# Optimization experiments

Hardware: AMD Instinct MI355X
Metric: run time of the kernel (lower is better)

The kernel has to match this reference:

```python
import jax, jax.numpy as jnp
import numpy as np

K = 16      # n_sample neighbors
L = 2       # stacked PT blocks
D = 128     # in_dim
H = 128     # hidden_dim = out_dim = vector_dim
EPS = 1e-5


def _bn(x, g, b, axes):
    # batch-norm with batch statistics (train-mode MinkowskiBatchNorm / BN1d / BN2d)
    m = jnp.mean(x, axes, keepdims=True)
    v = jnp.var(x, axes, keepdims=True)
    return (x - m) * jax.lax.rsqrt(v + EPS) * g + b


def setup_inputs():
    key = jax.random.key(0)
    ks = jax.random.split(key, 16)
    B, Nper = 2, 8192
    coords = jax.random.randint(ks[0], (B, Nper, 3), 0, 200, dtype=jnp.int32)
    feats = jax.random.normal(ks[1], (B * Nper, D), dtype=jnp.float32)
    w = lambda k, s: jax.random.normal(k, s, dtype=jnp.float32) * 0.1
    return {
        'coords': coords, 'feats': feats,
        'W_top': w(ks[2], (L, D, H)),
        'bn_top_g': jnp.ones((L, H)), 'bn_top_b': jnp.zeros((L, H)),
        'W_phi': w(ks[3], (L, H, H)),
        'W_psi': w(ks[4], (L, H, H)),
        'W_alpha': w(ks[5], (L, H, H)),
        'W_d1': w(ks[6], (L, 3, H)), 'b_d1': jnp.zeros((L, H)),
        'bn_d1_g': jnp.ones((L, H)), 'bn_d1_b': jnp.zeros((L, H)),
        'W_d2': w(ks[7], (L, H, H)), 'b_d2': jnp.zeros((L, H)),
        'bn_d2_g': jnp.ones((L, H)), 'bn_d2_b': jnp.zeros((L, H)),
        'W_g1': w(ks[8], (L, H, H)), 'b_g1': jnp.zeros((L, H)),
        'bn_g1_g': jnp.ones((L, H)), 'bn_g1_b': jnp.zeros((L, H)),
        'W_g2': w(ks[9], (L, H, H)), 'b_g2': jnp.zeros((L, H)),
        'bn_g2_g': jnp.ones((L, H)), 'bn_g2_b': jnp.zeros((L, H)),
        'W_down': w(ks[10], (L, H, D)),
        'bn_down_g': jnp.ones((L, D)), 'bn_down_b': jnp.zeros((L, D)),
    }


def _knn(coords):
    # cube_query with USE_KNN=True: per-scene KNN grouping (self included)
    cf = coords.astype(jnp.float32)

    def one(c):  # c: (Nper, 3)
        d2 = jnp.sum((c[:, None, :] - c[None, :, :]) ** 2, -1)  # (Nper, Nper)
        _, idx = jax.lax.top_k(-d2, K)
        return idx

    idx = jax.vmap(one)(cf)                      # (B, Nper, K) per-scene indices
    nbr = jax.vmap(lambda c, i: c[i])(cf, idx)   # (B, Nper, K, 3) grouped coords
    rel = nbr - cf[:, :, None, :]                # relative xyz (pose input)
    B, Nper = coords.shape[0], coords.shape[1]
    gidx = (idx + (jnp.arange(B, dtype=idx.dtype) * Nper)[:, None, None]).reshape(-1, K)
    return rel.reshape(-1, K, 3), gidx           # (N,K,3), (N,K) global indices


def reference(coords, feats, W_top, bn_top_g, bn_top_b, W_phi, W_psi, W_alpha,
              W_d1, b_d1, bn_d1_g, bn_d1_b, W_d2, b_d2, bn_d2_g, bn_d2_b,
              W_g1, b_g1, bn_g1_g, bn_g1_b, W_g2, b_g2, bn_g2_g, bn_g2_b,
              W_down, bn_down_g, bn_down_b):
    rel, gidx = _knn(coords)
    f = feats
    for l in range(L):
        h = _bn(f @ W_top[l], bn_top_g[l], bn_top_b[l], 0)  # linear_top (1x1 conv + BN)
        # delta: pointwise MLP 3 -> H -> H on relative xyz (position encoding)
        pose = jax.nn.relu(_bn(rel @ W_d1[l] + b_d1[l], bn_d1_g[l], bn_d1_b[l], (0, 1)))
        pose = _bn(pose @ W_d2[l] + b_d2[l], bn_d2_g[l], bn_d2_b[l], (0, 1))  # (N,K,H)
        q = h @ W_phi[l]               # (N, H)
        kk = (h @ W_psi[l])[gidx]      # neighbor keys   (N, K, H)
        v = (h @ W_alpha[l])[gidx]     # neighbor values (N, K, H)
        # gamma: pointwise MLP on (phi - psi + pose), vector attention logits
        a = q[:, None, :] - kk + pose
        a = jax.nn.relu(_bn(a @ W_g1[l] + b_g1[l], bn_g1_g[l], bn_g1_b[l], (0, 1)))
        a = _bn(a @ W_g2[l] + b_g2[l], bn_g2_g[l], bn_g2_b[l], (0, 1))
        attn = jax.nn.softmax(a, axis=1)          # per-channel softmax over K neighbors
        y = jnp.sum(attn * (v + pose), axis=1)    # (N, H) vector-attention aggregation
        y = _bn(y @ W_down[l], bn_down_g[l], bn_down_b[l], 0)  # linear_down + BN
        f = y + f                                  # residual
    return f
```

## Files before the change

### kernel.cpp

```cpp
#include <hip/hip_runtime.h>

using u16 = unsigned short;
using u32 = unsigned int;
using u64 = unsigned long long;

#define NPTS   16384
#define NPER   8192
#define KNN    16
#define NKROWS (NPTS*KNN)
#define HD     128
#define CAP    160

typedef _Float16 half8 __attribute__((ext_vector_type(8)));
typedef float    floatx4 __attribute__((ext_vector_type(4)));

__device__ __forceinline__ u16  f2h(float f){ _Float16 h=(_Float16)f; return __builtin_bit_cast(u16,h); }
__device__ __forceinline__ float h2f(u16 u){ return (float)__builtin_bit_cast(_Float16,u); }
__device__ __forceinline__ u32 umin32(u32 a,u32 b){ return a<b?a:b; }

__global__ __launch_bounds__(256) void pack_coords(const int* __restrict__ coords, u32* __restrict__ pc){
    int i = blockIdx.x*256 + threadIdx.x;
    pc[i] = (u32)coords[3*i] | ((u32)coords[3*i+1]<<8) | ((u32)coords[3*i+2]<<16);
}

struct WPtrs { const float* p[8]; };
__global__ __launch_bounds__(256) void prep_weights(WPtrs wp, u16* __restrict__ wt){
    int idx = blockIdx.x*256 + threadIdx.x;
    int t = idx>>15, rem = idx&32767;
    int l = rem>>14, e = rem&16383;
    int n = e>>7, k = e&127;
    wt[idx] = f2h(wp.p[t][l*16384 + k*128 + n]);
}

__global__ __launch_bounds__(256) void knn2(const u32* __restrict__ pc, int* __restrict__ idx_g,
                                            float* __restrict__ rel, u64* __restrict__ sM){
    __shared__ u32 sc[NPER];
    __shared__ u32 buf[4][CAP];
    __shared__ u64 red[9];
    int tid = threadIdx.x;
    int wave = tid>>6, lane = tid&63;
    int scene = blockIdx.x >> 11;
    int q = (blockIdx.x & 2047)*4 + wave;

    const uint4* s4 = (const uint4*)(pc + scene*NPER);
#pragma unroll
    for (int i=0;i<8;i++) ((uint4*)sc)[tid + i*256] = s4[tid + i*256];
    if (tid<9) red[tid]=0;
    if (lane<16) buf[wave][lane]=0xFFFFFFFFu;
    __syncthreads();

    u32 qp = sc[q];
    int qx=(int)(qp&255), qy=(int)((qp>>8)&255), qz=(int)((qp>>16)&255);
    u32 thresh = 0xFFFFFFFFu;
    u32 cnt = 16;

    auto merge = [&](){
        u32 v0 = (lane      < (int)cnt) ? buf[wave][lane]      : 0xFFFFFFFFu;
        u32 v1 = (lane+64   < (int)cnt) ? buf[wave][lane+64]   : 0xFFFFFFFFu;
        u32 v2 = (lane+128  < (int)cnt) ? buf[wave][lane+128]  : 0xFFFFFFFFu;
        u32 out = 0;
#pragma unroll
        for (int r=0;r<16;r++){
            u32 m = umin32(umin32(v0,v1),v2);
#pragma unroll
            for (int o=32;o>=1;o>>=1) m = umin32(m, (u32)__shfl_xor((int)m, o, 64));
            if      (v0==m) v0=0xFFFFFFFFu;
            else if (v1==m) v1=0xFFFFFFFFu;
            else if (v2==m) v2=0xFFFFFFFFu;
            if (lane==r) out = m;
            thresh = m;
        }
        if (lane<16) buf[wave][lane] = out;
        cnt = 16;
    };

    for (int t=0;t<128;t++){
        u32 p = sc[t*64+lane];
        int dx=(int)(p&255)-qx, dy=(int)((p>>8)&255)-qy, dz=(int)((p>>16)&255)-qz;
        u32 d2 = (u32)(__mul24(dx,dx)+__mul24(dy,dy)+__mul24(dz,dz));
        u32 key = (d2<<13) | (u32)(t*64+lane);
        u64 mask = __ballot(key < thresh);
        if (mask){
            u32 lt = __builtin_amdgcn_mbcnt_hi((u32)(mask>>32), __builtin_amdgcn_mbcnt_lo((u32)mask,0));
            if (key < thresh) buf[wave][cnt + lt] = key;
            cnt += (u32)__popcll(mask);
            if (cnt > CAP-64) merge();
        }
    }
    merge();

    int n = scene*NPER + q;
    u32 key = buf[wave][lane & 15];
    int dx=0,dy=0,dz=0;
    if (lane<16){
        int j = (int)(key & 8191u);
        idx_g[(size_t)n*KNN + lane] = scene*NPER + j;
        u32 p = sc[j];
        dx=(int)(p&255)-qx; dy=(int)((p>>8)&255)-qy; dz=(int)((p>>16)&255)-qz;
        size_t ro = ((size_t)n*KNN+lane)*3;
        rel[ro]=(float)dx; rel[ro+1]=(float)dy; rel[ro+2]=(float)dz;
    }
    int arr[9] = {dx,dy,dz, dx*dx,dy*dy,dz*dz, dx*dy,dx*dz,dy*dz};
#pragma unroll
    for (int o=32;o>=1;o>>=1)
#pragma unroll
        for (int j=0;j<9;j++) arr[j] += __shfl_xor(arr[j], o, 64);
    if (lane==0)
#pragma unroll
        for (int j=0;j<9;j++) atomicAdd(&red[j], (u64)(long long)arr[j]);
    __syncthreads();
    if (tid<9) atomicAdd(&sM[tid], red[tid]);
}

__global__ __launch_bounds__(256) void finalize_d1(const u64* __restrict__ sM, const float* __restrict__ W_d1,
        const float* __restrict__ b_d1, const float* __restrict__ g, const float* __restrict__ beta,
        float* __restrict__ A, float* __restrict__ C){
    int tid=threadIdx.x; int l=tid>>7, c=tid&127;
    double s0=(double)(long long)sM[0], s1=(double)(long long)sM[1], s2=(double)(long long)sM[2];
    double m00=(double)(long long)sM[3], m11=(double)(long long)sM[4], m22=(double)(long long)sM[5];
    double m01=(double)(long long)sM[6], m02=(double)(long long)sM[7], m12=(double)(long long)sM[8];
    double w0=W_d1[l*384+c], w1=W_d1[l*384+128+c], w2=W_d1[l*384+256+c];
    double b =b_d1[l*128+c];
    double S = s0*w0+s1*w1+s2*w2;
    double Q = m00*w0*w0+m11*w1*w1+m22*w2*w2 + 2.0*(m01*w0*w1+m02*w0*w2+m12*w1*w2);
    double cnt = (double)NKROWS;
    double mean = S/cnt + b;
    double ex2  = (Q + 2.0*b*S)/cnt + b*b;
    double var  = ex2 - mean*mean;
    float a = g[l*128+c] * (float)(1.0/sqrt(var+1e-5));
    A[l*128+c]=a; C[l*128+c]=beta[l*128+c]-(float)mean*a;
}

__global__ void finalize_affine(double* __restrict__ P, const float* __restrict__ g,
        const float* __restrict__ b, double cnt, float* __restrict__ A, float* __restrict__ C){
    int c=threadIdx.x;
    double s=0.0, q=0.0;
    for (int k=0;k<64;k++){
        s+=P[k*256+c]; q+=P[k*256+128+c];
        P[k*256+c]=0.0; P[k*256+128+c]=0.0;
    }
    double mean=s/cnt, var=q/cnt-mean*mean;
    float a = g[c] * (float)(1.0/sqrt(var+1e-5));
    A[c]=a; C[c]=b[c]-(float)mean*a;
}

struct CompF32 {
    const float* src;
    __device__ __forceinline__ void stage(u16* As,int R0,int k0,int tid) const {
#pragma unroll
        for (int u=0;u<8;u++){
            int flat=u*256+tid, row=flat>>4, c4=flat&15; int k=k0+c4*4;
            const float4 v=*(const float4*)(src+(size_t)(R0+row)*HD+k);
            ushort4 o; o.x=f2h(v.x); o.y=f2h(v.y); o.z=f2h(v.z); o.w=f2h(v.w);
            *(ushort4*)(As+row*72+c4*4)=o;
        }
    }
};
struct CompH16Aff {
    const u16* src; const float* Aa; const float* Ca;
    __device__ __forceinline__ void stage(u16* As,int R0,int k0,int tid) const {
#pragma unroll
        for (int u=0;u<8;u++){
            int flat=u*256+tid, row=flat>>4, c4=flat&15; int k=k0+c4*4;
            const ushort4 v=*(const ushort4*)(src+(size_t)(R0+row)*HD+k);
            ushort4 o;
            o.x=f2h(h2f(v.x)*Aa[k]  +Ca[k]);   o.y=f2h(h2f(v.y)*Aa[k+1]+Ca[k+1]);
            o.z=f2h(h2f(v.z)*Aa[k+2]+Ca[k+2]); o.w=f2h(h2f(v.w)*Aa[k+3]+Ca[k+3]);
            *(ushort4*)(As+row*72+c4*4)=o;
        }
    }
};
struct CompH16AffRelu {
    const u16* src; const float* Aa; const float* Ca;
    __device__ __forceinline__ void stage(u16* As,int R0,int k0,int tid) const {
#pragma unroll
        for (int u=0;u<8;u++){
            int flat=u*256+tid, row=flat>>4, c4=flat&15; int k=k0+c4*4;
            const ushort4 v=*(const ushort4*)(src+(size_t)(R0+row)*HD+k);
            ushort4 o;
            o.x=f2h(fmaxf(h2f(v.x)*Aa[k]  +Ca[k],  0.f));
            o.y=f2h(fmaxf(h2f(v.y)*Aa[k+1]+Ca[k+1],0.f));
            o.z=f2h(fmaxf(h2f(v.z)*Aa[k+2]+Ca[k+2],0.f));
            o.w=f2h(fmaxf(h2f(v.w)*Aa[k+3]+Ca[k+3],0.f));
            *(ushort4*)(As+row*72+c4*4)=o;
        }
    }
};
struct CompPose1 {
    const float* rel; const float* Wd1; const float* bd1; const float* Aa; const float* Ca;
    __device__ __forceinline__ void stage(u16* As,int R0,int k0,int tid) const {
#pragma unroll
        for (int u=0;u<8;u++){
            int flat=u*256+tid, row=flat>>4, c4=flat&15; int k=k0+c4*4; int R=R0+row;
            float r0=rel[(size_t)R*3], r1=rel[(size_t)R*3+1], r2=rel[(size_t)R*3+2];
            ushort4 o;
#pragma unroll
            for (int j=0;j<4;j++){
                int kk=k+j;
                float x = r0*Wd1[kk] + r1*Wd1[HD+kk] + r2*Wd1[2*HD+kk] + bd1[kk];
                x = fmaxf(x*Aa[kk]+Ca[kk], 0.f);
                ((u16*)&o)[j]=f2h(x);
            }
            *(ushort4*)(As+row*72+c4*4)=o;
        }
    }
};
struct CompA0 {
    const u16* q; const u16* kp; const u16* pose; const int* gidx; const float* Aa; const float* Ca;
    __device__ __forceinline__ void stage(u16* As,int R0,int k0,int tid) const {
#pragma unroll
        for (int u=0;u<8;u++){
            int flat=u*256+tid, row=flat>>4, c4=flat&15; int k=k0+c4*4; int R=R0+row;
            int n=R>>4; int g=gidx[R];
            const ushort4 qv=*(const ushort4*)(q +(size_t)n*HD+k);
            const ushort4 kv=*(const ushort4*)(kp+(size_t)g*HD+k);
            const ushort4 pv=*(const ushort4*)(pose+(size_t)R*HD+k);
            ushort4 o;
            o.x=f2h(h2f(qv.x)-h2f(kv.x) + h2f(pv.x)*Aa[k]  +Ca[k]);
            o.y=f2h(h2f(qv.y)-h2f(kv.y) + h2f(pv.y)*Aa[k+1]+Ca[k+1]);
            o.z=f2h(h2f(qv.z)-h2f(kv.z) + h2f(pv.z)*Aa[k+2]+Ca[k+2]);
            o.w=f2h(h2f(qv.w)-h2f(kv.w) + h2f(pv.w)*Aa[k+3]+Ca[k+3]);
            *(ushort4*)(As+row*72+c4*4)=o;
        }
    }
};

template<class Comp, bool OUT16, bool HASBIAS, bool STATS>
__global__ __launch_bounds__(256) void gemm128(Comp comp, const u16* __restrict__ Wt,
        const float* __restrict__ bias, void* __restrict__ outp, double* __restrict__ statsP){
    __shared__ __align__(16) u16 As[128*72];
    __shared__ __align__(16) u16 Bs[128*72];
    __shared__ float cs2[2][128], cq2[2][128];
    int tid=threadIdx.x;
    int R0=blockIdx.x*128;
    int lane=tid&63, wave=tid>>6, quad=lane>>4, r16=lane&15;
    int wm=wave>>1, wn=wave&1;
    floatx4 acc[4][4]={};
#pragma unroll
    for (int ks=0;ks<2;ks++){
        int k0=ks*64;
        comp.stage(As,R0,k0,tid);
#pragma unroll
        for (int u=0;u<4;u++){
            int flat=u*256+tid, n=flat>>3, c8=flat&7;
            *(int4*)(Bs+n*72+c8*8) = *(const int4*)(Wt+n*HD+k0+c8*8);
        }
        __syncthreads();
#pragma unroll
        for (int kk2=0;kk2<2;kk2++){
            half8 aF[4], bF[4];
#pragma unroll
            for (int mi=0;mi<4;mi++) aF[mi]=*(const half8*)(As+(wm*64+mi*16+r16)*72 + kk2*32+quad*8);
#pragma unroll
            for (int ni=0;ni<4;ni++) bF[ni]=*(const half8*)(Bs+(wn*64+ni*16+r16)*72 + kk2*32+quad*8);
#pragma unroll
            for (int mi=0;mi<4;mi++)
#pragma unroll
                for (int ni=0;ni<4;ni++)
                    acc[mi][ni]=__builtin_amdgcn_mfma_f32_16x16x32_f16(aF[mi],bF[ni],acc[mi][ni],0,0,0);
        }
        __syncthreads();
    }
    float sAcc[4]={0,0,0,0}, qAcc[4]={0,0,0,0};
#pragma unroll
    for (int mi=0;mi<4;mi++)
#pragma unroll
        for (int ni=0;ni<4;ni++){
            int col=wn*64+ni*16+r16;
            float bv = HASBIAS ? bias[col] : 0.f;
#pragma unroll
            for (int rg=0;rg<4;rg++){
                int row=R0+wm*64+mi*16+quad*4+rg;
                float v=acc[mi][ni][rg]+bv;
                if (STATS){ sAcc[ni]+=v; qAcc[ni]+=v*v; }
                if (OUT16) ((u16*)outp)[(size_t)row*HD+col]=f2h(v);
                else       ((float*)outp)[(size_t)row*HD+col]=v;
            }
        }
    if (STATS){
#pragma unroll
        for (int ni=0;ni<4;ni++){
            float s=sAcc[ni], q=qAcc[ni];
            s += __shfl_xor(s,16,64); s += __shfl_xor(s,32,64);
            q += __shfl_xor(q,16,64); q += __shfl_xor(q,32,64);
            if (quad==0){
                int col=wn*64+ni*16+r16;
                cs2[wm][col]=s; cq2[wm][col]=q;
            }
        }
        __syncthreads();
        if (tid<128){
            int slot = blockIdx.x & 63;
            unsafeAtomicAdd(&statsP[slot*256+tid],     (double)(cs2[0][tid]+cs2[1][tid]));
            unsafeAtomicAdd(&statsP[slot*256+128+tid], (double)(cq2[0][tid]+cq2[1][tid]));
        }
    }
}

__global__ __launch_bounds__(256) void aggregate(const u16* __restrict__ a2, const u16* __restrict__ pose,
        const u16* __restrict__ vv, const int* __restrict__ gidx,
        const float* __restrict__ Ag2, const float* __restrict__ Cg2,
        const float* __restrict__ Ad2, const float* __restrict__ Cd2, float* __restrict__ y){
    int c=threadIdx.x&127, h=threadIdx.x>>7;
    int n=blockIdx.x*2+h;
    float sA=Ag2[c], sC=Cg2[c], pA=Ad2[c], pC=Cd2[c];
    float av[16]; float m=-1e30f;
#pragma unroll
    for (int k=0;k<16;k++){ float a=h2f(a2[((size_t)n*16+k)*HD+c])*sA+sC; av[k]=a; m=fmaxf(m,a); }
    float sum=0.f;
#pragma unroll
    for (int k=0;k<16;k++){ float e=__expf(av[k]-m); av[k]=e; sum+=e; }
    float acc=0.f;
#pragma unroll
    for (int k=0;k<16;k++){
        int g=gidx[n*16+k];
        float pv = h2f(pose[((size_t)n*16+k)*HD+c])*pA+pC + h2f(vv[(size_t)g*HD+c]);
        acc += av[k]*pv;
    }
    y[(size_t)n*HD+c]=acc/sum;
}

__global__ __launch_bounds__(256) void residual(const float* __restrict__ ydown, const float* __restrict__ A,
        const float* __restrict__ C, const float* __restrict__ fin, float* __restrict__ fout){
    size_t i=(size_t)blockIdx.x*256+threadIdx.x; int c=(int)(i&127);
    fout[i]=ydown[i]*A[c]+C[c]+fin[i];
}

extern "C" void kernel_launch(void* const* d_in, const int* in_sizes, int n_in,
                              void* d_out, int out_size, void* d_ws, size_t ws_size,
                              hipStream_t stream){
    const int*   coords=(const int*)d_in[0];
    const float* feats=(const float*)d_in[1];
    const float* W_top=(const float*)d_in[2];
    const float* g_top=(const float*)d_in[3];
    const float* bt_top=(const float*)d_in[4];
    const float* W_phi=(const float*)d_in[5];
    const float* W_psi=(const float*)d_in[6];
    const float* W_alp=(const float*)d_in[7];
    const float* W_d1=(const float*)d_in[8];
    const float* b_d1=(const float*)d_in[9];
    const float* g_d1=(const float*)d_in[10];
    const float* bt_d1=(const float*)d_in[11];
    const float* W_d2=(const float*)d_in[12];
    const float* b_d2=(const float*)d_in[13];
    const float* g_d2=(const float*)d_in[14];
    const float* bt_d2=(const float*)d_in[15];
    const float* W_g1=(const float*)d_in[16];
    const float* b_g1=(const float*)d_in[17];
    const float* g_g1=(const float*)d_in[18];
    const float* bt_g1=(const float*)d_in[19];
    const float* W_g2=(const float*)d_in[20];
    const float* b_g2=(const float*)d_in[21];
    const float* g_g2=(const float*)d_in[22];
    const float* bt_g2=(const float*)d_in[23];
    const float* W_dn=(const float*)d_in[24];
    const float* g_dn=(const float*)d_in[25];
    const float* bt_dn=(const float*)d_in[26];

    char* ws=(char*)d_ws;
    size_t off=0;
    auto carve=[&](size_t bytes)->char*{ char* p=ws+off; off=(off+bytes+255)&~(size_t)255; return p; };
    u32*    pc    =(u32*)   carve((size_t)NPTS*4);
    int*    idxg  =(int*)   carve((size_t)NKROWS*4);
    float*  rel   =(float*) carve((size_t)NKROWS*3*4);
    u16*    h16   =(u16*)   carve((size_t)NPTS*HD*2);
    u16*    qb    =(u16*)   carve((size_t)NPTS*HD*2);
    u16*    kpb   =(u16*)   carve((size_t)NPTS*HD*2);
    u16*    vvb   =(u16*)   carve((size_t)NPTS*HD*2);
    float*  yb    =(float*) carve((size_t)NPTS*HD*4);
    float*  ydown =(float*) carve((size_t)NPTS*HD*4);
    float*  fbuf  =(float*) carve((size_t)NPTS*HD*4);
    u16*    wt    =(u16*)   carve((size_t)8*2*16384*2);
    char*   stats =         carve(64*256*8 + 256);
    double* P     =(double*)stats;
    u64*    sM    =(u64*)(stats + 64*256*8);
    float*  aff   =(float*) carve(8192);
    float *A_top=aff, *C_top=aff+128, *A_d2=aff+256, *C_d2=aff+384,
          *A_g1=aff+512, *C_g1=aff+640, *A_g2=aff+768, *C_g2=aff+896,
          *A_dn=aff+1024, *C_dn=aff+1152, *A_d1=aff+1280, *C_d1=aff+1536;
    u16*    pose2 =(u16*)   carve((size_t)NKROWS*HD*2);
    u16*    abuf  =(u16*)   carve((size_t)NKROWS*HD*2);
    if (ws_size < off) return;

    hipMemsetAsync(stats, 0, 64*256*8 + 256, stream);
    pack_coords<<<dim3(NPTS/256),dim3(256),0,stream>>>(coords, pc);
    WPtrs wp{{W_top,W_phi,W_psi,W_alp,W_d2,W_g1,W_g2,W_dn}};
    prep_weights<<<dim3(8*2*16384/256),dim3(256),0,stream>>>(wp, wt);
    knn2<<<dim3(4096),dim3(256),0,stream>>>(pc, idxg, rel, sM);
    finalize_d1<<<dim3(1),dim3(256),0,stream>>>(sM, W_d1, b_d1, g_d1, bt_d1, A_d1, C_d1);

    const float* fin=feats;
    for (int l=0;l<2;l++){
        const u16* wt_top=wt+(0*2+l)*16384; const u16* wt_phi=wt+(1*2+l)*16384;
        const u16* wt_psi=wt+(2*2+l)*16384; const u16* wt_alp=wt+(3*2+l)*16384;
        const u16* wt_d2 =wt+(4*2+l)*16384; const u16* wt_g1 =wt+(5*2+l)*16384;
        const u16* wt_g2 =wt+(6*2+l)*16384; const u16* wt_dn =wt+(7*2+l)*16384;

        gemm128<CompF32,true,false,true><<<dim3(NPTS/128),dim3(256),0,stream>>>(CompF32{fin}, wt_top, nullptr, h16, P);
        finalize_affine<<<dim3(1),dim3(128),0,stream>>>(P, g_top+l*128, bt_top+l*128, (double)NPTS, A_top, C_top);

        gemm128<CompH16Aff,true,false,false><<<dim3(NPTS/128),dim3(256),0,stream>>>(CompH16Aff{h16,A_top,C_top}, wt_phi, nullptr, qb, nullptr);
        gemm128<CompH16Aff,true,false,false><<<dim3(NPTS/128),dim3(256),0,stream>>>(CompH16Aff{h16,A_top,C_top}, wt_psi, nullptr, kpb, nullptr);
        gemm128<CompH16Aff,true,false,false><<<dim3(NPTS/128),dim3(256),0,stream>>>(CompH16Aff{h16,A_top,C_top}, wt_alp, nullptr, vvb, nullptr);

        gemm128<CompPose1,true,true,true><<<dim3(NKROWS/128),dim3(256),0,stream>>>(
            CompPose1{rel, W_d1+l*384, b_d1+l*128, A_d1+l*128, C_d1+l*128}, wt_d2, b_d2+l*128, pose2, P);
        finalize_affine<<<dim3(1),dim3(128),0,stream>>>(P, g_d2+l*128, bt_d2+l*128, (double)NKROWS, A_d2, C_d2);

        gemm128<CompA0,true,true,true><<<dim3(NKROWS/128),dim3(256),0,stream>>>(
            CompA0{qb,kpb,pose2,idxg,A_d2,C_d2}, wt_g1, b_g1+l*128, abuf, P);
        finalize_affine<<<dim3(1),dim3(128),0,stream>>>(P, g_g1+l*128, bt_g1+l*128, (double)NKROWS, A_g1, C_g1);

        gemm128<CompH16AffRelu,true,true,true><<<dim3(NKROWS/128),dim3(256),0,stream>>>(
            CompH16AffRelu{abuf,A_g1,C_g1}, wt_g2, b_g2+l*128, abuf, P);
        finalize_affine<<<dim3(1),dim3(128),0,stream>>>(P, g_g2+l*128, bt_g2+l*128, (double)NKROWS, A_g2, C_g2);

        aggregate<<<dim3(NPTS/2),dim3(256),0,stream>>>(abuf, pose2, vvb, idxg, A_g2, C_g2, A_d2, C_d2, yb);

        gemm128<CompF32,false,false,true><<<dim3(NPTS/128),dim3(256),0,stream>>>(CompF32{yb}, wt_dn, nullptr, ydown, P);
        finalize_affine<<<dim3(1),dim3(128),0,stream>>>(P, g_dn+l*128, bt_dn+l*128, (double)NPTS, A_dn, C_dn);
        residual<<<dim3(NPTS*HD/256),dim3(256),0,stream>>>(ydown, A_dn, C_dn, fin, (l==1)?(float*)d_out:fbuf);
        fin=fbuf;
    }
}
```

Before: 638.3 us.

## Rework KNN loop, batch QKV GEMMs, vectorize aggregate, shrink stat slots

```diff
diff --git a/kernel.cpp b/kernel.cpp
--- a/kernel.cpp
+++ b/kernel.cpp
@@ -9,7 +9,8 @@
 #define KNN    16
 #define NKROWS (NPTS*KNN)
 #define HD     128
-#define CAP    160
+#define CAP    208
+#define NSLOT  16
 
 typedef _Float16 half8 __attribute__((ext_vector_type(8)));
 typedef float    floatx4 __attribute__((ext_vector_type(4)));
@@ -32,19 +33,19 @@
     wt[idx] = f2h(wp.p[t][l*16384 + k*128 + n]);
 }
 
-__global__ __launch_bounds__(256) void knn2(const u32* __restrict__ pc, int* __restrict__ idx_g,
+__global__ __launch_bounds__(512) void knn3(const u32* __restrict__ pc, int* __restrict__ idx_g,
                                             float* __restrict__ rel, u64* __restrict__ sM){
     __shared__ u32 sc[NPER];
-    __shared__ u32 buf[4][CAP];
+    __shared__ u32 buf[8][CAP];
     __shared__ u64 red[9];
     int tid = threadIdx.x;
     int wave = tid>>6, lane = tid&63;
-    int scene = blockIdx.x >> 11;
-    int q = (blockIdx.x & 2047)*4 + wave;
+    int scene = blockIdx.x >> 10;
+    int q = (blockIdx.x & 1023)*8 + wave;
 
     const uint4* s4 = (const uint4*)(pc + scene*NPER);
 #pragma unroll
-    for (int i=0;i<8;i++) ((uint4*)sc)[tid + i*256] = s4[tid + i*256];
+    for (int i=0;i<4;i++) ((uint4*)sc)[tid + i*512] = s4[tid + i*512];
     if (tid<9) red[tid]=0;
     if (lane<16) buf[wave][lane]=0xFFFFFFFFu;
     __syncthreads();
@@ -58,15 +59,17 @@
         u32 v0 = (lane      < (int)cnt) ? buf[wave][lane]      : 0xFFFFFFFFu;
         u32 v1 = (lane+64   < (int)cnt) ? buf[wave][lane+64]   : 0xFFFFFFFFu;
         u32 v2 = (lane+128  < (int)cnt) ? buf[wave][lane+128]  : 0xFFFFFFFFu;
+        u32 v3 = (lane+192  < (int)cnt) ? buf[wave][lane+192]  : 0xFFFFFFFFu;
         u32 out = 0;
 #pragma unroll
         for (int r=0;r<16;r++){
-            u32 m = umin32(umin32(v0,v1),v2);
+            u32 m = umin32(umin32(v0,v1),umin32(v2,v3));
 #pragma unroll
             for (int o=32;o>=1;o>>=1) m = umin32(m, (u32)__shfl_xor((int)m, o, 64));
             if      (v0==m) v0=0xFFFFFFFFu;
             else if (v1==m) v1=0xFFFFFFFFu;
             else if (v2==m) v2=0xFFFFFFFFu;
+            else if (v3==m) v3=0xFFFFFFFFu;
             if (lane==r) out = m;
             thresh = m;
         }
@@ -74,18 +77,33 @@
         cnt = 16;
     };
 
-    for (int t=0;t<128;t++){
-        u32 p = sc[t*64+lane];
-        int dx=(int)(p&255)-qx, dy=(int)((p>>8)&255)-qy, dz=(int)((p>>16)&255)-qz;
-        u32 d2 = (u32)(__mul24(dx,dx)+__mul24(dy,dy)+__mul24(dz,dz));
-        u32 key = (d2<<13) | (u32)(t*64+lane);
-        u64 mask = __ballot(key < thresh);
-        if (mask){
-            u32 lt = __builtin_amdgcn_mbcnt_hi((u32)(mask>>32), __builtin_amdgcn_mbcnt_lo((u32)mask,0));
-            if (key < thresh) buf[wave][cnt + lt] = key;
-            cnt += (u32)__popcll(mask);
-            if (cnt > CAP-64) merge();
-        }
+    int lane2 = lane*2;
+    uint2 p2 = ((const uint2*)sc)[lane];
+    for (int t=0;t<64;t++){
+        uint2 cur = p2;
+        if (t<63) p2 = ((const uint2*)sc)[(t+1)*64+lane];
+        int base = t*128 + lane2;
+        u32 pa = cur.x;
+        int dx0=(int)(pa&255)-qx, dy0=(int)((pa>>8)&255)-qy, dz0=(int)((pa>>16)&255)-qz;
+        u32 d2_0 = (u32)(__mul24(dx0,dx0)+__mul24(dy0,dy0)+__mul24(dz0,dz0));
+        u32 key0 = (d2_0<<13) + (u32)base;
+        u32 pb = cur.y;
+        int dx1=(int)(pb&255)-qx, dy1=(int)((pb>>8)&255)-qy, dz1=(int)((pb>>16)&255)-qz;
+        u32 d2_1 = (u32)(__mul24(dx1,dx1)+__mul24(dy1,dy1)+__mul24(dz1,dz1));
+        u32 key1 = (d2_1<<13) + (u32)(base+1);
+        u64 m0 = __ballot(key0 < thresh);
+        if (m0){
+            u32 lt = __builtin_amdgcn_mbcnt_hi((u32)(m0>>32), __builtin_amdgcn_mbcnt_lo((u32)m0,0));
+            if (key0 < thresh) buf[wave][cnt + lt] = key0;
+            cnt += (u32)__popcll(m0);
+        }
+        u64 m1 = __ballot(key1 < thresh);
+        if (m1){
+            u32 lt = __builtin_amdgcn_mbcnt_hi((u32)(m1>>32), __builtin_amdgcn_mbcnt_lo((u32)m1,0));
+            if (key1 < thresh) buf[wave][cnt + lt] = key1;
+            cnt += (u32)__popcll(m1);
+        }
+        if (cnt > CAP-128) merge();
     }
     merge();
 
@@ -135,7 +153,8 @@
         const float* __restrict__ b, double cnt, float* __restrict__ A, float* __restrict__ C){
     int c=threadIdx.x;
     double s=0.0, q=0.0;
-    for (int k=0;k<64;k++){
+#pragma unroll
+    for (int k=0;k<NSLOT;k++){
         s+=P[k*256+c]; q+=P[k*256+128+c];
         P[k*256+c]=0.0; P[k*256+128+c]=0.0;
     }
@@ -227,10 +246,14 @@
 
 template<class Comp, bool OUT16, bool HASBIAS, bool STATS>
 __global__ __launch_bounds__(256) void gemm128(Comp comp, const u16* __restrict__ Wt,
-        const float* __restrict__ bias, void* __restrict__ outp, double* __restrict__ statsP){
+        const float* __restrict__ bias, void* __restrict__ outp, double* __restrict__ statsP,
+        int wtStride, long outStride){
     __shared__ __align__(16) u16 As[128*72];
     __shared__ __align__(16) u16 Bs[128*72];
     __shared__ float cs2[2][128], cq2[2][128];
+    const u16* W = Wt + (size_t)blockIdx.y*wtStride;
+    u16*   o16 = (u16*)outp   + (size_t)blockIdx.y*outStride;
+    float* o32 = (float*)outp + (size_t)blockIdx.y*outStride;
     int tid=threadIdx.x;
     int R0=blockIdx.x*128;
     int lane=tid&63, wave=tid>>6, quad=lane>>4, r16=lane&15;
@@ -243,7 +266,7 @@
 #pragma unroll
         for (int u=0;u<4;u++){
             int flat=u*256+tid, n=flat>>3, c8=flat&7;
-            *(int4*)(Bs+n*72+c8*8) = *(const int4*)(Wt+n*HD+k0+c8*8);
+            *(int4*)(Bs+n*72+c8*8) = *(const int4*)(W+n*HD+k0+c8*8);
         }
         __syncthreads();
 #pragma unroll
@@ -273,8 +296,8 @@
                 int row=R0+wm*64+mi*16+quad*4+rg;
                 float v=acc[mi][ni][rg]+bv;
                 if (STATS){ sAcc[ni]+=v; qAcc[ni]+=v*v; }
-                if (OUT16) ((u16*)outp)[(size_t)row*HD+col]=f2h(v);
-                else       ((float*)outp)[(size_t)row*HD+col]=v;
+                if (OUT16) o16[(size_t)row*HD+col]=f2h(v);
+                else       o32[(size_t)row*HD+col]=v;
             }
         }
     if (STATS){
@@ -290,7 +313,7 @@
         }
         __syncthreads();
         if (tid<128){
-            int slot = blockIdx.x & 63;
+            int slot = blockIdx.x & (NSLOT-1);
             unsafeAtomicAdd(&statsP[slot*256+tid],     (double)(cs2[0][tid]+cs2[1][tid]));
             unsafeAtomicAdd(&statsP[slot*256+128+tid], (double)(cq2[0][tid]+cq2[1][tid]));
         }
@@ -301,23 +324,34 @@
         const u16* __restrict__ vv, const int* __restrict__ gidx,
         const float* __restrict__ Ag2, const float* __restrict__ Cg2,
         const float* __restrict__ Ad2, const float* __restrict__ Cd2, float* __restrict__ y){
-    int c=threadIdx.x&127, h=threadIdx.x>>7;
-    int n=blockIdx.x*2+h;
-    float sA=Ag2[c], sC=Cg2[c], pA=Ad2[c], pC=Cd2[c];
-    float av[16]; float m=-1e30f;
-#pragma unroll
-    for (int k=0;k<16;k++){ float a=h2f(a2[((size_t)n*16+k)*HD+c])*sA+sC; av[k]=a; m=fmaxf(m,a); }
-    float sum=0.f;
-#pragma unroll
-    for (int k=0;k<16;k++){ float e=__expf(av[k]-m); av[k]=e; sum+=e; }
-    float acc=0.f;
+    int c=(threadIdx.x&63)*2, h=threadIdx.x>>6;
+    int n=blockIdx.x*4+h;
+    float sA0=Ag2[c], sC0=Cg2[c], pA0=Ad2[c], pC0=Cd2[c];
+    float sA1=Ag2[c+1], sC1=Cg2[c+1], pA1=Ad2[c+1], pC1=Cd2[c+1];
+    float av0[16], av1[16]; float m0=-1e30f, m1=-1e30f;
+#pragma unroll
+    for (int k=0;k<16;k++){
+        ushort2 t=*(const ushort2*)(a2+((size_t)n*16+k)*HD+c);
+        float a0=h2f(t.x)*sA0+sC0, a1=h2f(t.y)*sA1+sC1;
+        av0[k]=a0; av1[k]=a1; m0=fmaxf(m0,a0); m1=fmaxf(m1,a1);
+    }
+    float sum0=0.f, sum1=0.f;
+#pragma unroll
+    for (int k=0;k<16;k++){
+        float e0=__expf(av0[k]-m0), e1=__expf(av1[k]-m1);
+        av0[k]=e0; av1[k]=e1; sum0+=e0; sum1+=e1;
+    }
+    float acc0=0.f, acc1=0.f;
 #pragma unroll
     for (int k=0;k<16;k++){
         int g=gidx[n*16+k];
-        float pv = h2f(pose[((size_t)n*16+k)*HD+c])*pA+pC + h2f(vv[(size_t)g*HD+c]);
-        acc += av[k]*pv;
-    }
-    y[(size_t)n*HD+c]=acc/sum;
+        ushort2 pt=*(const ushort2*)(pose+((size_t)n*16+k)*HD+c);
+        ushort2 vt=*(const ushort2*)(vv+(size_t)g*HD+c);
+        acc0 += av0[k]*(h2f(pt.x)*pA0+pC0 + h2f(vt.x));
+        acc1 += av1[k]*(h2f(pt.y)*pA1+pC1 + h2f(vt.y));
+    }
+    y[(size_t)n*HD+c]  =acc0/sum0;
+    y[(size_t)n*HD+c+1]=acc1/sum1;
 }
 
 __global__ __launch_bounds__(256) void residual(const float* __restrict__ ydown, const float* __restrict__ A,
@@ -364,16 +398,16 @@
     int*    idxg  =(int*)   carve((size_t)NKROWS*4);
     float*  rel   =(float*) carve((size_t)NKROWS*3*4);
     u16*    h16   =(u16*)   carve((size_t)NPTS*HD*2);
-    u16*    qb    =(u16*)   carve((size_t)NPTS*HD*2);
-    u16*    kpb   =(u16*)   carve((size_t)NPTS*HD*2);
-    u16*    vvb   =(u16*)   carve((size_t)NPTS*HD*2);
+    u16*    qb    =(u16*)   carve((size_t)3*NPTS*HD*2);
+    u16*    kpb   = qb + (size_t)NPTS*HD;
+    u16*    vvb   = qb + (size_t)2*NPTS*HD;
     float*  yb    =(float*) carve((size_t)NPTS*HD*4);
     float*  ydown =(float*) carve((size_t)NPTS*HD*4);
     float*  fbuf  =(float*) carve((size_t)NPTS*HD*4);
     u16*    wt    =(u16*)   carve((size_t)8*2*16384*2);
-    char*   stats =         carve(64*256*8 + 256);
+    char*   stats =         carve(NSLOT*256*8 + 256);
     double* P     =(double*)stats;
-    u64*    sM    =(u64*)(stats + 64*256*8);
+    u64*    sM    =(u64*)(stats + NSLOT*256*8);
     float*  aff   =(float*) carve(8192);
     float *A_top=aff, *C_top=aff+128, *A_d2=aff+256, *C_d2=aff+384,
           *A_g1=aff+512, *C_g1=aff+640, *A_g2=aff+768, *C_g2=aff+896,
@@ -382,42 +416,42 @@
     u16*    abuf  =(u16*)   carve((size_t)NKROWS*HD*2);
     if (ws_size < off) return;
 
-    hipMemsetAsync(stats, 0, 64*256*8 + 256, stream);
+    hipMemsetAsync(stats, 0, NSLOT*256*8 + 256, stream);
     pack_coords<<<dim3(NPTS/256),dim3(256),0,stream>>>(coords, pc);
     WPtrs wp{{W_top,W_phi,W_psi,W_alp,W_d2,W_g1,W_g2,W_dn}};
     prep_weights<<<dim3(8*2*16384/256),dim3(256),0,stream>>>(wp, wt);
-    knn2<<<dim3(4096),dim3(256),0,stream>>>(pc, idxg, rel, sM);
+    knn3<<<dim3(2048),dim3(512),0,stream>>>(pc, idxg, rel, sM);
     finalize_d1<<<dim3(1),dim3(256),0,stream>>>(sM, W_d1, b_d1, g_d1, bt_d1, A_d1, C_d1);
 
     const float* fin=feats;
     for (int l=0;l<2;l++){
         const u16* wt_top=wt+(0*2+l)*16384; const u16* wt_phi=wt+(1*2+l)*16384;
-        const u16* wt_psi=wt+(2*2+l)*16384; const u16* wt_alp=wt+(3*2+l)*16384;
         const u16* wt_d2 =wt+(4*2+l)*16384; const u16* wt_g1 =wt+(5*2+l)*16384;
         const u16* wt_g2 =wt+(6*2+l)*16384; const u16* wt_dn =wt+(7*2+l)*16384;
 
-        gemm128<CompF32,true,false,true><<<dim3(NPTS/128),dim3(256),0,stream>>>(CompF32{fin}, wt_top, nullptr, h16, P);
+        gemm128<CompF32,true,false,true><<<dim3(NPTS/128),dim3(256),0,stream>>>(
+            CompF32{fin}, wt_top, nullptr, h16, P, 0, 0);
         finalize_affine<<<dim3(1),dim3(128),0,stream>>>(P, g_top+l*128, bt_top+l*128, (double)NPTS, A_top, C_top);
 
-        gemm128<CompH16Aff,true,false,false><<<dim3(NPTS/128),dim3(256),0,stream>>>(CompH16Aff{h16,A_top,C_top}, wt_phi, nullptr, qb, nullptr);
-        gemm128<CompH16Aff,true,false,false><<<dim3(NPTS/128),dim3(256),0,stream>>>(CompH16Aff{h16,A_top,C_top}, wt_psi, nullptr, kpb, nullptr);
-        gemm128<CompH16Aff,true,false,false><<<dim3(NPTS/128),dim3(256),0,stream>>>(CompH16Aff{h16,A_top,C_top}, wt_alp, nullptr, vvb, nullptr);
+        gemm128<CompH16Aff,true,false,false><<<dim3(NPTS/128,3),dim3(256),0,stream>>>(
+            CompH16Aff{h16,A_top,C_top}, wt_phi, nullptr, qb, nullptr, 2*16384, (long)NPTS*HD);
 
         gemm128<CompPose1,true,true,true><<<dim3(NKROWS/128),dim3(256),0,stream>>>(
-            CompPose1{rel, W_d1+l*384, b_d1+l*128, A_d1+l*128, C_d1+l*128}, wt_d2, b_d2+l*128, pose2, P);
+            CompPose1{rel, W_d1+l*384, b_d1+l*128, A_d1+l*128, C_d1+l*128}, wt_d2, b_d2+l*128, pose2, P, 0, 0);
         finalize_affine<<<dim3(1),dim3(128),0,stream>>>(P, g_d2+l*128, bt_d2+l*128, (double)NKROWS, A_d2, C_d2);
 
         gemm128<CompA0,true,true,true><<<dim3(NKROWS/128),dim3(256),0,stream>>>(
-            CompA0{qb,kpb,pose2,idxg,A_d2,C_d2}, wt_g1, b_g1+l*128, abuf, P);
+            CompA0{qb,kpb,pose2,idxg,A_d2,C_d2}, wt_g1, b_g1+l*128, abuf, P, 0, 0);
         finalize_affine<<<dim3(1),dim3(128),0,stream>>>(P, g_g1+l*128, bt_g1+l*128, (double)NKROWS, A_g1, C_g1);
 
         gemm128<CompH16AffRelu,true,true,true><<<dim3(NKROWS/128),dim3(256),0,stream>>>(
-            CompH16AffRelu{abuf,A_g1,C_g1}, wt_g2, b_g2+l*128, abuf, P);
+            CompH16AffRelu{abuf,A_g1,C_g1}, wt_g2, b_g2+l*128, abuf, P, 0, 0);
         finalize_affine<<<dim3(1),dim3(128),0,stream>>>(P, g_g2+l*128, bt_g2+l*128, (double)NKROWS, A_g2, C_g2);
 
-        aggregate<<<dim3(NPTS/2),dim3(256),0,stream>>>(abuf, pose2, vvb, idxg, A_g2, C_g2, A_d2, C_d2, yb);
-
-        gemm128<CompF32,false,false,true><<<dim3(NPTS/128),dim3(256),0,stream>>>(CompF32{yb}, wt_dn, nullptr, ydown, P);
+        aggregate<<<dim3(NPTS/4),dim3(256),0,stream>>>(abuf, pose2, vvb, idxg, A_g2, C_g2, A_d2, C_d2, yb);
+
+        gemm128<CompF32,false,false,true><<<dim3(NPTS/128),dim3(256),0,stream>>>(
+            CompF32{yb}, wt_dn, nullptr, ydown, P, 0, 0);
         finalize_affine<<<dim3(1),dim3(128),0,stream>>>(P, g_dn+l*128, bt_dn+l*128, (double)NPTS, A_dn, C_dn);
         residual<<<dim3(NPTS*HD/256),dim3(256),0,stream>>>(ydown, A_dn, C_dn, fin, (l==1)?(float*)d_out:fbuf);
         fin=fbuf;
```

New measurement: 559.5 us. -12.3%, faster.
